# Performance work log

Hardware: AMD Instinct MI355X
Metric: run time of the kernel (lower is better)

The kernel has to match this reference:

```python
import jax, jax.numpy as jnp
import numpy as np

B, LQ, LK, D, H, DK = 128, 32, 128, 1024, 16, 64


def setup_inputs() -> dict:
    key = jax.random.key(0)
    ks = jax.random.split(key, 10)
    Q_seq = jax.random.normal(ks[0], (B, LQ, D), dtype=jnp.float32)
    K_seq = jax.random.normal(ks[1], (B, LK, D), dtype=jnp.float32)
    V_seq = jax.random.normal(ks[2], (B, LK, D), dtype=jnp.float32)
    title_mask = (jax.random.uniform(ks[3], (B, LQ)) < 0.9).astype(jnp.float32)
    body_mask = (jax.random.uniform(ks[4], (B, LQ, LK)) < 0.9).astype(jnp.float32)
    s = 1.0 / np.sqrt(D)
    Wq = jax.random.uniform(ks[5], (H * DK, D), jnp.float32, -s, s)
    Wk = jax.random.uniform(ks[6], (H * DK, D), jnp.float32, -s, s)
    Wv = jax.random.uniform(ks[7], (H * DK, D), jnp.float32, -s, s)
    bq = jnp.zeros((H * DK,), jnp.float32)
    bk = jnp.zeros((H * DK,), jnp.float32)
    bv = jnp.zeros((H * DK,), jnp.float32)
    return {"Q_seq": Q_seq, "K_seq": K_seq, "V_seq": V_seq,
            "title_mask": title_mask, "body_mask": body_mask,
            "Wq": Wq, "bq": bq, "Wk": Wk, "bk": bk, "Wv": Wv, "bv": bv}


def reference(Q_seq, K_seq, V_seq, title_mask, body_mask, Wq, bq, Wk, bk, Wv, bv):
    b = Q_seq.shape[0]
    # concatenate title tokens onto keys/values: [B, LK+LQ, D]
    K_cat = jnp.concatenate([K_seq, Q_seq], axis=1)
    V_cat = jnp.concatenate([V_seq, Q_seq], axis=1)
    # mask: [B, LQ, LK+LQ]
    tmask_rep = jnp.broadcast_to(title_mask[:, None, :], (b, LQ, LQ))
    mask = jnp.concatenate([body_mask, tmask_rep], axis=2) * title_mask[:, :, None]
    # projections -> [B, H, len, DK]
    Qh = (Q_seq @ Wq.T + bq).reshape(b, LQ, H, DK).transpose(0, 2, 1, 3)
    Kh = (K_cat @ Wk.T + bk).reshape(b, LK + LQ, H, DK).transpose(0, 2, 1, 3)
    Vh = (V_cat @ Wv.T + bv).reshape(b, LK + LQ, H, DK).transpose(0, 2, 1, 3)
    # custom exp-based masked attention (non-softmax normalization)
    scores = jnp.einsum('bhqd,bhkd->bhqk', Qh, Kh) / np.sqrt(float(DK))
    scores = jnp.exp(scores) * mask[:, None, :, :]
    attn = scores / (jnp.sum(scores, axis=-1, keepdims=True) + 1e-8)
    ctx = jnp.einsum('bhqk,bhkd->bhqd', attn, Vh)
    return ctx.transpose(0, 2, 1, 3).reshape(b, LQ, H * DK)
```

## Files before the change

kernel.cpp:

```cpp
#include <hip/hip_runtime.h>

typedef _Float16 f16;
typedef _Float16 f16x2 __attribute__((ext_vector_type(2)));
typedef _Float16 f16x4 __attribute__((ext_vector_type(4)));
typedef _Float16 f16x8 __attribute__((ext_vector_type(8)));
typedef float f32x4v __attribute__((ext_vector_type(4)));

#define AS1 __attribute__((address_space(1)))
#define AS3 __attribute__((address_space(3)))

__device__ __forceinline__ void gload_lds16(const f16* g, f16* l) {
  __builtin_amdgcn_global_load_lds((const AS1 unsigned int*)g,
                                   (AS3 unsigned int*)l, 16, 0, 0);
}

__global__ __launch_bounds__(256) void prep_kernel(
    const float* __restrict__ Q_seq, const float* __restrict__ K_seq,
    const float* __restrict__ V_seq,
    const float* __restrict__ Wq, const float* __restrict__ Wk,
    const float* __restrict__ Wv,
    f16* __restrict__ Qb, f16* __restrict__ Kb, f16* __restrict__ Vb,
    f16* __restrict__ Wqb, f16* __restrict__ Wkb, f16* __restrict__ Wvb)
{
  const long long g = (long long)blockIdx.x * 256 + threadIdx.x;
  const float* s;
  f16* d;
  if (g < 1048576) {
    s = Q_seq + g * 4; d = Qb + g * 4;
  } else if (g < 5242880) {
    long long e = (g - 1048576) * 4; s = K_seq + e; d = Kb + e;
  } else if (g < 9437184) {
    long long e = (g - 5242880) * 4; s = V_seq + e; d = Vb + e;
  } else if (g < 9699328) {
    long long e = (g - 9437184) * 4; s = Wq + e; d = Wqb + e;
  } else if (g < 9961472) {
    long long e = (g - 9699328) * 4; s = Wk + e; d = Wkb + e;
  } else {
    long long e = (g - 9961472) * 4; s = Wv + e; d = Wvb + e;
  }
  float4 v = *(const float4*)s;
  f16x4 o;
  o.x = (f16)v.x; o.y = (f16)v.y; o.z = (f16)v.z; o.w = (f16)v.w;
  *(f16x4*)d = o;
}

__device__ __forceinline__ void gemm_tile_128(
    const f16* __restrict__ A, const f16* __restrict__ W,
    const float* __restrict__ bias, f16* __restrict__ C,
    int m0, int n0, int rowShift, int outStride, int rowOff,
    f16* As, f16* Bs)
{
  const int t = threadIdx.x;
  const int w = t >> 6, lane = t & 63;
  const int wr = w >> 1, wc = w & 1;
  const int sr = lane >> 2, sc = (lane & 3) * 8;

  const f16* gA0 = A + (long long)(m0 + (w * 2 + 0) * 16 + sr) * 1024 + sc;
  const f16* gA1 = A + (long long)(m0 + (w * 2 + 1) * 16 + sr) * 1024 + sc;
  const f16* gB0 = W + (long long)(n0 + (w * 2 + 0) * 16 + sr) * 1024 + sc;
  const f16* gB1 = W + (long long)(n0 + (w * 2 + 1) * 16 + sr) * 1024 + sc;
  f16* lA0 = As + (w * 2 + 0) * 512;
  f16* lA1 = As + (w * 2 + 1) * 512;
  f16* lB0 = Bs + (w * 2 + 0) * 512;
  f16* lB1 = Bs + (w * 2 + 1) * 512;

  f32x4v acc[4][4];
#pragma unroll
  for (int i = 0; i < 4; ++i)
#pragma unroll
    for (int j = 0; j < 4; ++j) acc[i][j] = (f32x4v){0.f, 0.f, 0.f, 0.f};

  const int fr = lane & 15;
  const int fk = (lane >> 4) * 8;
  const f16* pA = As + (wr * 64 + fr) * 32 + fk;
  const f16* pB = Bs + (wc * 64 + fr) * 32 + fk;

  for (int k0 = 0; k0 < 1024; k0 += 32) {
    gload_lds16(gA0 + k0, lA0);
    gload_lds16(gA1 + k0, lA1);
    gload_lds16(gB0 + k0, lB0);
    gload_lds16(gB1 + k0, lB1);
    __syncthreads();
    f16x8 av[4], bv[4];
#pragma unroll
    for (int i = 0; i < 4; ++i) av[i] = *(const f16x8*)(pA + i * 16 * 32);
#pragma unroll
    for (int i = 0; i < 4; ++i) bv[i] = *(const f16x8*)(pB + i * 16 * 32);
#pragma unroll
    for (int i = 0; i < 4; ++i)
#pragma unroll
      for (int j = 0; j < 4; ++j)
        acc[i][j] = __builtin_amdgcn_mfma_f32_16x16x32_f16(av[i], bv[j],
                                                           acc[i][j], 0, 0, 0);
    __syncthreads();
  }

  const int rowMask = (1 << rowShift) - 1;
  float bn[4];
#pragma unroll
  for (int j = 0; j < 4; ++j) bn[j] = bias[n0 + wc * 64 + j * 16 + fr];
#pragma unroll
  for (int i = 0; i < 4; ++i) {
#pragma unroll
    for (int j = 0; j < 4; ++j) {
#pragma unroll
      for (int v = 0; v < 4; ++v) {
        int arow = m0 + wr * 64 + i * 16 + (lane >> 4) * 4 + v;
        int orow = (arow >> rowShift) * outStride + (arow & rowMask) + rowOff;
        int col = n0 + wc * 64 + j * 16 + fr;
        C[(long long)orow * 1024 + col] = (f16)(acc[i][j][v] + bn[j]);
      }
    }
  }
}

__global__ __launch_bounds__(256) void gemm_kv(
    const f16* __restrict__ A, const f16* __restrict__ W,
    const float* __restrict__ bias, f16* __restrict__ C)
{
  __shared__ __align__(16) f16 As[128 * 32];
  __shared__ __align__(16) f16 Bs[128 * 32];
  gemm_tile_128(A, W, bias, C, blockIdx.y * 128, blockIdx.x * 128,
                7, 160, 0, As, Bs);
}

__global__ __launch_bounds__(256) void gemm_q3(
    const f16* __restrict__ Qb,
    const f16* __restrict__ Wqb, const f16* __restrict__ Wkb,
    const f16* __restrict__ Wvb,
    const float* __restrict__ bq, const float* __restrict__ bk,
    const float* __restrict__ bv,
    f16* __restrict__ Qh, f16* __restrict__ Kh, f16* __restrict__ Vh)
{
  __shared__ __align__(16) f16 As[128 * 32];
  __shared__ __align__(16) f16 Bs[128 * 32];
  const int z = blockIdx.z;
  const f16* W = (z == 0) ? Wqb : (z == 1) ? Wkb : Wvb;
  const float* bias = (z == 0) ? bq : (z == 1) ? bk : bv;
  f16* C = (z == 0) ? Qh : (z == 1) ? Kh : Vh;
  const int outStride = (z == 0) ? 32 : 160;
  const int rowOff = (z == 0) ? 0 : 128;
  gemm_tile_128(Qb, W, bias, C, blockIdx.y * 128, blockIdx.x * 128,
                5, outStride, rowOff, As, Bs);
}

__global__ __launch_bounds__(256) void attn_kernel(
    const f16* __restrict__ Qh, const f16* __restrict__ Kh,
    const f16* __restrict__ Vh,
    const float* __restrict__ title, const float* __restrict__ body,
    float* __restrict__ out)
{
  __shared__ __align__(16) f16 Qs[32 * 72];
  __shared__ __align__(16) f16 Ks[160 * 72];
  __shared__ __align__(16) f16 Vs[160 * 68];
  __shared__ float rs[4][32];
  __shared__ float invs[32];

  const int bh = blockIdx.x, b = bh >> 4, h = bh & 15;
  const int t = threadIdx.x, w = t >> 6, lane = t & 63;
  const int c = lane & 15, g = lane >> 4;

  const long long qbase = ((long long)(b * 32) << 10) + h * 64;
  const long long kbase = ((long long)(b * 160) << 10) + h * 64;

  {
    int row = t >> 3, ch = t & 7;
    *(f16x8*)(Qs + row * 72 + ch * 8) =
        *(const f16x8*)(Qh + qbase + (long long)row * 1024 + ch * 8);
  }
#pragma unroll
  for (int r = 0; r < 5; ++r) {
    int i = t + r * 256;
    int row = i >> 3, ch = i & 7;
    *(f16x8*)(Ks + row * 72 + ch * 8) =
        *(const f16x8*)(Kh + kbase + (long long)row * 1024 + ch * 8);
    f16x8 vv = *(const f16x8*)(Vh + kbase + (long long)row * 1024 + ch * 8);
    f16x4 vlo = __builtin_shufflevector(vv, vv, 0, 1, 2, 3);
    f16x4 vhi = __builtin_shufflevector(vv, vv, 4, 5, 6, 7);
    *(f16x4*)(Vs + row * 68 + ch * 8) = vlo;
    *(f16x4*)(Vs + row * 68 + ch * 8 + 4) = vhi;
  }
  __syncthreads();

  f16x8 qf[2][2];
#pragma unroll
  for (int qt = 0; qt < 2; ++qt)
#pragma unroll
    for (int s = 0; s < 2; ++s)
      qf[qt][s] = *(const f16x8*)(Qs + (qt * 16 + c) * 72 + s * 32 + g * 8);

  const int cnt = (w < 2) ? 3 : 2;
  const int tile0 = (w < 2) ? w * 3 : 6 + (w - 2) * 2;

  f16x4 pp[3][2];
  float rsum[2] = {0.f, 0.f};

#pragma unroll
  for (int i = 0; i < 3; ++i) {
    if (i < cnt) {
      const int kt = tile0 + i;
      f16x8 kf0 = *(const f16x8*)(Ks + (kt * 16 + c) * 72 + 0 + g * 8);
      f16x8 kf1 = *(const f16x8*)(Ks + (kt * 16 + c) * 72 + 32 + g * 8);
#pragma unroll
      for (int qt = 0; qt < 2; ++qt) {
        f32x4v s4 = (f32x4v){0.f, 0.f, 0.f, 0.f};
        s4 = __builtin_amdgcn_mfma_f32_16x16x32_f16(kf0, qf[qt][0], s4, 0, 0, 0);
        s4 = __builtin_amdgcn_mfma_f32_16x16x32_f16(kf1, qf[qt][1], s4, 0, 0, 0);
        float4 m4;
        if (kt < 8) {
          m4 = *(const float4*)(body +
                ((long long)(b * 32 + qt * 16 + c)) * 128 + kt * 16 + 4 * g);
        } else {
          m4 = *(const float4*)(title + b * 32 + (kt - 8) * 16 + 4 * g);
        }
        float e0 = __expf(s4[0] * 0.125f) * m4.x;
        float e1 = __expf(s4[1] * 0.125f) * m4.y;
        float e2 = __expf(s4[2] * 0.125f) * m4.z;
        float e3 = __expf(s4[3] * 0.125f) * m4.w;
        rsum[qt] += (e0 + e1) + (e2 + e3);
        f16x4 p4;
        p4.x = (f16)e0; p4.y = (f16)e1; p4.z = (f16)e2; p4.w = (f16)e3;
        pp[i][qt] = p4;
      }
    }
  }

#pragma unroll
  for (int qt = 0; qt < 2; ++qt) {
    rsum[qt] += __shfl_xor(rsum[qt], 16);
    rsum[qt] += __shfl_xor(rsum[qt], 32);
  }
  if (lane < 16) {
    rs[w][c] = rsum[0];
    rs[w][16 + c] = rsum[1];
  }
  __syncthreads();

  f16* Ps = Ks;
#pragma unroll
  for (int i = 0; i < 3; ++i) {
    if (i < cnt) {
      const int kt = tile0 + i;
#pragma unroll
      for (int qt = 0; qt < 2; ++qt)
        *(f16x4*)(Ps + (qt * 16 + c) * 168 + kt * 16 + 4 * g) = pp[i][qt];
    }
  }
  if (t < 32) {
    float ssum = rs[0][t] + rs[1][t] + rs[2][t] + rs[3][t];
    invs[t] = title[b * 32 + t] / (ssum + 1e-8f);
  }
  __syncthreads();

  f32x4v o[2] = {(f32x4v){0.f, 0.f, 0.f, 0.f}, (f32x4v){0.f, 0.f, 0.f, 0.f}};
#pragma unroll
  for (int s = 0; s < 5; ++s) {
    f16x8 vf;
#pragma unroll
    for (int j = 0; j < 8; ++j)
      vf[j] = Vs[(32 * s + 8 * g + j) * 68 + 16 * w + c];
#pragma unroll
    for (int qt = 0; qt < 2; ++qt) {
      f16x8 pf = *(const f16x8*)(Ps + (qt * 16 + c) * 168 + s * 32 + g * 8);
      o[qt] = __builtin_amdgcn_mfma_f32_16x16x32_f16(pf, vf, o[qt], 0, 0, 0);
    }
  }

#pragma unroll
  for (int qt = 0; qt < 2; ++qt) {
#pragma unroll
    for (int v = 0; v < 4; ++v) {
      int q = qt * 16 + 4 * g + v;
      out[((long long)(b * 32 + q) << 10) + h * 64 + 16 * w + c] =
          o[qt][v] * invs[q];
    }
  }
}

extern "C" void kernel_launch(void* const* d_in, const int* in_sizes, int n_in,
                              void* d_out, int out_size, void* d_ws, size_t ws_size,
                              hipStream_t stream) {
  const float* Q_seq = (const float*)d_in[0];
  const float* K_seq = (const float*)d_in[1];
  const float* V_seq = (const float*)d_in[2];
  const float* title = (const float*)d_in[3];
  const float* body  = (const float*)d_in[4];
  const float* Wq = (const float*)d_in[5];
  const float* bq = (const float*)d_in[6];
  const float* Wk = (const float*)d_in[7];
  const float* bk = (const float*)d_in[8];
  const float* Wv = (const float*)d_in[9];
  const float* bv = (const float*)d_in[10];
  float* out = (float*)d_out;

  f16* ws = (f16*)d_ws;
  f16* Qb  = ws;
  f16* Kb  = Qb + 4194304;
  f16* Vb  = Kb + 16777216;
  f16* Wqb = Vb + 16777216;
  f16* Wkb = Wqb + 1048576;
  f16* Wvb = Wkb + 1048576;
  f16* Qh  = Wvb + 1048576;
  f16* Kh  = Qh + 4194304;
  f16* Vh  = Kh + 20971520;

  prep_kernel<<<39936, 256, 0, stream>>>(Q_seq, K_seq, V_seq, Wq, Wk, Wv,
                                         Qb, Kb, Vb, Wqb, Wkb, Wvb);
  gemm_kv<<<dim3(8, 128), 256, 0, stream>>>(Kb, Wkb, bk, Kh);
  gemm_kv<<<dim3(8, 128), 256, 0, stream>>>(Vb, Wvb, bv, Vh);
  gemm_q3<<<dim3(8, 32, 3), 256, 0, stream>>>(Qb, Wqb, Wkb, Wvb, bq, bk, bv,
                                              Qh, Kh, Vh);
  attn_kernel<<<2048, 256, 0, stream>>>(Qh, Kh, Vh, title, body, out);
}
```

Before: 216.5 us.

## Widen GEMM K-step, stage epilogue through LDS, merge K/V GEMM launches

The GEMM tile now loads two 32-wide K slices per iteration, which halves the number of barrier pairs. The epilogue writes the accumulator tile into padded shared memory and then stores it to global memory as coalesced 16-byte rows instead of scattered 2-byte writes. The two K/V projection launches are merged into a single launch with a z dimension, and the prep kernel converts 8 floats per thread instead of 4. Shared memory per block grows to about 34KB, which may reduce occupancy.

```diff
diff --git a/kernel.cpp b/kernel.cpp
--- a/kernel.cpp
+++ b/kernel.cpp
@@ -25,44 +25,51 @@
   const long long g = (long long)blockIdx.x * 256 + threadIdx.x;
   const float* s;
   f16* d;
-  if (g < 1048576) {
-    s = Q_seq + g * 4; d = Qb + g * 4;
-  } else if (g < 5242880) {
-    long long e = (g - 1048576) * 4; s = K_seq + e; d = Kb + e;
-  } else if (g < 9437184) {
-    long long e = (g - 5242880) * 4; s = V_seq + e; d = Vb + e;
-  } else if (g < 9699328) {
-    long long e = (g - 9437184) * 4; s = Wq + e; d = Wqb + e;
-  } else if (g < 9961472) {
-    long long e = (g - 9699328) * 4; s = Wk + e; d = Wkb + e;
+  if (g < 524288) {
+    s = Q_seq + g * 8; d = Qb + g * 8;
+  } else if (g < 2621440) {
+    long long e = (g - 524288) * 8; s = K_seq + e; d = Kb + e;
+  } else if (g < 4718592) {
+    long long e = (g - 2621440) * 8; s = V_seq + e; d = Vb + e;
+  } else if (g < 4849664) {
+    long long e = (g - 4718592) * 8; s = Wq + e; d = Wqb + e;
+  } else if (g < 4980736) {
+    long long e = (g - 4849664) * 8; s = Wk + e; d = Wkb + e;
   } else {
-    long long e = (g - 9961472) * 4; s = Wv + e; d = Wvb + e;
-  }
-  float4 v = *(const float4*)s;
-  f16x4 o;
-  o.x = (f16)v.x; o.y = (f16)v.y; o.z = (f16)v.z; o.w = (f16)v.w;
-  *(f16x4*)d = o;
+    long long e = (g - 4980736) * 8; s = Wv + e; d = Wvb + e;
+  }
+  float4 v0 = *(const float4*)s;
+  float4 v1 = *(const float4*)(s + 4);
+  f16x8 o;
+  o[0] = (f16)v0.x; o[1] = (f16)v0.y; o[2] = (f16)v0.z; o[3] = (f16)v0.w;
+  o[4] = (f16)v1.x; o[5] = (f16)v1.y; o[6] = (f16)v1.z; o[7] = (f16)v1.w;
+  *(f16x8*)d = o;
 }
 
 __device__ __forceinline__ void gemm_tile_128(
     const f16* __restrict__ A, const f16* __restrict__ W,
     const float* __restrict__ bias, f16* __restrict__ C,
     int m0, int n0, int rowShift, int outStride, int rowOff,
-    f16* As, f16* Bs)
-{
+    f16* sbuf)
+{
+  f16* As0 = sbuf;
+  f16* As1 = sbuf + 4096;
+  f16* Bs0 = sbuf + 8192;
+  f16* Bs1 = sbuf + 12288;
+
   const int t = threadIdx.x;
   const int w = t >> 6, lane = t & 63;
   const int wr = w >> 1, wc = w & 1;
   const int sr = lane >> 2, sc = (lane & 3) * 8;
 
-  const f16* gA0 = A + (long long)(m0 + (w * 2 + 0) * 16 + sr) * 1024 + sc;
-  const f16* gA1 = A + (long long)(m0 + (w * 2 + 1) * 16 + sr) * 1024 + sc;
-  const f16* gB0 = W + (long long)(n0 + (w * 2 + 0) * 16 + sr) * 1024 + sc;
-  const f16* gB1 = W + (long long)(n0 + (w * 2 + 1) * 16 + sr) * 1024 + sc;
-  f16* lA0 = As + (w * 2 + 0) * 512;
-  f16* lA1 = As + (w * 2 + 1) * 512;
-  f16* lB0 = Bs + (w * 2 + 0) * 512;
-  f16* lB1 = Bs + (w * 2 + 1) * 512;
+  const f16* gA0 = A + (long long)(m0 + w * 32 + sr) * 1024 + sc;
+  const f16* gA1 = A + (long long)(m0 + w * 32 + 16 + sr) * 1024 + sc;
+  const f16* gB0 = W + (long long)(n0 + w * 32 + sr) * 1024 + sc;
+  const f16* gB1 = W + (long long)(n0 + w * 32 + 16 + sr) * 1024 + sc;
+  f16* lA0 = As0 + (w * 32) * 32;
+  f16* lA1 = As0 + (w * 32 + 16) * 32;
+  f16* lB0 = Bs0 + (w * 32) * 32;
+  f16* lB1 = Bs0 + (w * 32 + 16) * 32;
 
   f32x4v acc[4][4];
 #pragma unroll
@@ -72,56 +79,82 @@
 
   const int fr = lane & 15;
   const int fk = (lane >> 4) * 8;
-  const f16* pA = As + (wr * 64 + fr) * 32 + fk;
-  const f16* pB = Bs + (wc * 64 + fr) * 32 + fk;
-
-  for (int k0 = 0; k0 < 1024; k0 += 32) {
+  const f16* pA = As0 + (wr * 64 + fr) * 32 + fk;
+  const f16* pB = Bs0 + (wc * 64 + fr) * 32 + fk;
+
+  for (int k0 = 0; k0 < 1024; k0 += 64) {
     gload_lds16(gA0 + k0, lA0);
     gload_lds16(gA1 + k0, lA1);
+    gload_lds16(gA0 + k0 + 32, lA0 + 4096);
+    gload_lds16(gA1 + k0 + 32, lA1 + 4096);
     gload_lds16(gB0 + k0, lB0);
     gload_lds16(gB1 + k0, lB1);
+    gload_lds16(gB0 + k0 + 32, lB0 + 4096);
+    gload_lds16(gB1 + k0 + 32, lB1 + 4096);
     __syncthreads();
-    f16x8 av[4], bv[4];
-#pragma unroll
-    for (int i = 0; i < 4; ++i) av[i] = *(const f16x8*)(pA + i * 16 * 32);
-#pragma unroll
-    for (int i = 0; i < 4; ++i) bv[i] = *(const f16x8*)(pB + i * 16 * 32);
-#pragma unroll
-    for (int i = 0; i < 4; ++i)
-#pragma unroll
-      for (int j = 0; j < 4; ++j)
-        acc[i][j] = __builtin_amdgcn_mfma_f32_16x16x32_f16(av[i], bv[j],
-                                                           acc[i][j], 0, 0, 0);
+#pragma unroll
+    for (int kk = 0; kk < 2; ++kk) {
+      f16x8 av[4], bv[4];
+#pragma unroll
+      for (int i = 0; i < 4; ++i)
+        av[i] = *(const f16x8*)(pA + kk * 4096 + i * 16 * 32);
+#pragma unroll
+      for (int i = 0; i < 4; ++i)
+        bv[i] = *(const f16x8*)(pB + kk * 4096 + i * 16 * 32);
+#pragma unroll
+      for (int i = 0; i < 4; ++i)
+#pragma unroll
+        for (int j = 0; j < 4; ++j)
+          acc[i][j] = __builtin_amdgcn_mfma_f32_16x16x32_f16(av[i], bv[j],
+                                                             acc[i][j], 0, 0, 0);
+    }
     __syncthreads();
   }
 
+  f16* Cs = sbuf;
+  float bn[4];
+#pragma unroll
+  for (int j = 0; j < 4; ++j) bn[j] = bias[n0 + wc * 64 + j * 16 + fr];
+  const int g4 = (lane >> 4) * 4;
+#pragma unroll
+  for (int i = 0; i < 4; ++i) {
+#pragma unroll
+    for (int j = 0; j < 4; ++j) {
+#pragma unroll
+      for (int v = 0; v < 4; ++v) {
+        int row = wr * 64 + i * 16 + g4 + v;
+        int col = wc * 64 + j * 16 + fr;
+        Cs[row * 136 + col] = (f16)(acc[i][j][v] + bn[j]);
+      }
+    }
+  }
+  __syncthreads();
+
   const int rowMask = (1 << rowShift) - 1;
-  float bn[4];
-#pragma unroll
-  for (int j = 0; j < 4; ++j) bn[j] = bias[n0 + wc * 64 + j * 16 + fr];
-#pragma unroll
-  for (int i = 0; i < 4; ++i) {
-#pragma unroll
-    for (int j = 0; j < 4; ++j) {
-#pragma unroll
-      for (int v = 0; v < 4; ++v) {
-        int arow = m0 + wr * 64 + i * 16 + (lane >> 4) * 4 + v;
-        int orow = (arow >> rowShift) * outStride + (arow & rowMask) + rowOff;
-        int col = n0 + wc * 64 + j * 16 + fr;
-        C[(long long)orow * 1024 + col] = (f16)(acc[i][j][v] + bn[j]);
-      }
-    }
-  }
-}
-
-__global__ __launch_bounds__(256) void gemm_kv(
-    const f16* __restrict__ A, const f16* __restrict__ W,
-    const float* __restrict__ bias, f16* __restrict__ C)
-{
-  __shared__ __align__(16) f16 As[128 * 32];
-  __shared__ __align__(16) f16 Bs[128 * 32];
+  const int row = t >> 1, half = t & 1;
+  const int arow = m0 + row;
+  const int orow = (arow >> rowShift) * outStride + (arow & rowMask) + rowOff;
+  f16* dst = C + (long long)orow * 1024 + n0 + half * 64;
+  const f16* srcr = Cs + row * 136 + half * 64;
+#pragma unroll
+  for (int c = 0; c < 8; ++c)
+    *(f16x8*)(dst + c * 8) = *(const f16x8*)(srcr + c * 8);
+}
+
+__global__ __launch_bounds__(256) void gemm_kv2(
+    const f16* __restrict__ Kb, const f16* __restrict__ Wkb,
+    const float* __restrict__ bk, f16* __restrict__ Kh,
+    const f16* __restrict__ Vb, const f16* __restrict__ Wvb,
+    const float* __restrict__ bv, f16* __restrict__ Vh)
+{
+  __shared__ __align__(16) f16 sbuf[128 * 136];
+  const int z = blockIdx.z;
+  const f16* A = z ? Vb : Kb;
+  const f16* W = z ? Wvb : Wkb;
+  const float* bias = z ? bv : bk;
+  f16* C = z ? Vh : Kh;
   gemm_tile_128(A, W, bias, C, blockIdx.y * 128, blockIdx.x * 128,
-                7, 160, 0, As, Bs);
+                7, 160, 0, sbuf);
 }
 
 __global__ __launch_bounds__(256) void gemm_q3(
@@ -132,8 +165,7 @@
     const float* __restrict__ bv,
     f16* __restrict__ Qh, f16* __restrict__ Kh, f16* __restrict__ Vh)
 {
-  __shared__ __align__(16) f16 As[128 * 32];
-  __shared__ __align__(16) f16 Bs[128 * 32];
+  __shared__ __align__(16) f16 sbuf[128 * 136];
   const int z = blockIdx.z;
   const f16* W = (z == 0) ? Wqb : (z == 1) ? Wkb : Wvb;
   const float* bias = (z == 0) ? bq : (z == 1) ? bk : bv;
@@ -141,7 +173,7 @@
   const int outStride = (z == 0) ? 32 : 160;
   const int rowOff = (z == 0) ? 0 : 128;
   gemm_tile_128(Qb, W, bias, C, blockIdx.y * 128, blockIdx.x * 128,
-                5, outStride, rowOff, As, Bs);
+                5, outStride, rowOff, sbuf);
 }
 
 __global__ __launch_bounds__(256) void attn_kernel(
@@ -304,10 +336,10 @@
   f16* Kh  = Qh + 4194304;
   f16* Vh  = Kh + 20971520;
 
-  prep_kernel<<<39936, 256, 0, stream>>>(Q_seq, K_seq, V_seq, Wq, Wk, Wv,
+  prep_kernel<<<19968, 256, 0, stream>>>(Q_seq, K_seq, V_seq, Wq, Wk, Wv,
                                          Qb, Kb, Vb, Wqb, Wkb, Wvb);
-  gemm_kv<<<dim3(8, 128), 256, 0, stream>>>(Kb, Wkb, bk, Kh);
-  gemm_kv<<<dim3(8, 128), 256, 0, stream>>>(Vb, Wvb, bv, Vh);
+  gemm_kv2<<<dim3(8, 128, 2), 256, 0, stream>>>(Kb, Wkb, bk, Kh,
+                                                Vb, Wvb, bv, Vh);
   gemm_q3<<<dim3(8, 32, 3), 256, 0, stream>>>(Qb, Wqb, Wkb, Wvb, bq, bk, bv,
                                               Qh, Kh, Vh);
   attn_kernel<<<2048, 256, 0, stream>>>(Qh, Kh, Vh, title, body, out);
```

Measured after the change: 220.3 us. No clear change (+1.8%).
